# Kernel tuning notes

Measured on AMD Instinct MI355X. Metric: run time of the kernel, lower is better.

Reference implementation:

```python
import jax, jax.numpy as jnp
import numpy as np

EPS = 1e-5  # torch BatchNorm1d default eps


def _bn(h, scale, bias):
    # BatchNorm in training mode: biased variance over the node/edge dim.
    mu = h.mean(0)
    var = h.var(0)
    return (h - mu) * jax.lax.rsqrt(var + EPS) * scale + bias


def _segment_mean(msg, idx, n):
    s = jax.ops.segment_sum(msg, idx, num_segments=n)
    cnt = jax.ops.segment_sum(jnp.ones((msg.shape[0],), msg.dtype), idx, num_segments=n)
    return s / jnp.maximum(cnt, 1.0)[:, None]


def setup_inputs() -> dict:
    N, E, D, L = 50000, 800000, 64, 3
    key = jax.random.key(0)
    ks = jax.random.split(key, 7)
    return {
        "x": jax.random.normal(ks[0], (N, D), jnp.float32),
        "edge_attr": jax.random.normal(ks[1], (E, D), jnp.float32),
        "edge_index": jax.random.randint(ks[2], (2, E), 0, N, dtype=jnp.int32),
        "v_w": jax.random.normal(ks[3], (L, 4, D, D), jnp.float32) / np.sqrt(D),
        "v_b": jax.random.normal(ks[4], (L, 4, D), jnp.float32) * 0.02,
        "e_w": jax.random.normal(ks[5], (L, D, D), jnp.float32) / np.sqrt(D),
        "e_b": jax.random.normal(ks[6], (L, D), jnp.float32) * 0.02,
        "vbn_scale": jnp.ones((L, D), jnp.float32),
        "vbn_bias": jnp.zeros((L, D), jnp.float32),
        "ebn_scale": jnp.ones((L, D), jnp.float32),
        "ebn_bias": jnp.zeros((L, D), jnp.float32),
    }


def reference(x, edge_attr, edge_index, v_w, v_b, e_w, e_b,
              vbn_scale, vbn_bias, ebn_scale, ebn_bias):
    n = x.shape[0]
    dst = edge_index[0]  # aggregation target (scatter index)
    src = edge_index[1]  # neighbor node (gather index)
    num_layers = v_w.shape[0]
    w = edge_attr
    for l in range(num_layers):
        x0, w0 = x, w
        # Four node projections in one einsum: [4, N, D]
        xp = jnp.einsum('nd,kde->kne', x0, v_w[l]) + v_b[l][:, None, :]
        x1, x2, x3, x4 = xp[0], xp[1], xp[2], xp[3]
        # Anisotropic edge-gated message passing (vertex update)
        msg = jax.nn.sigmoid(w0) * x2[src]              # [E, D]
        agg = _segment_mean(msg, dst, n)                # [N, D]
        x = x0 + jax.nn.silu(_bn(x1 + agg, vbn_scale[l], vbn_bias[l]))
        # Edge update
        w1 = w0 @ e_w[l] + e_b[l]
        w = w0 + jax.nn.silu(_bn(w1 + x3[dst] + x4[src], ebn_scale[l], ebn_bias[l]))
    return x, w
```

## Files before the change

### kernel.cpp

```cpp
#include <hip/hip_runtime.h>
#include <hip/hip_bf16.h>
#include <math.h>

typedef __attribute__((ext_vector_type(8))) short bf16x8;
typedef __attribute__((ext_vector_type(4))) float f32x4;

__device__ __forceinline__ float bflo(unsigned u) { return __uint_as_float(u << 16); }
__device__ __forceinline__ float bfhi(unsigned u) { return __uint_as_float(u & 0xffff0000u); }
__device__ __forceinline__ unsigned packbf(float a, float b) {
    unsigned ua = __float_as_uint(a), ub = __float_as_uint(b);
    ua += 0x7fffu + ((ua >> 16) & 1u);
    ub += 0x7fffu + ((ub >> 16) & 1u);
    return (ua >> 16) | (ub & 0xffff0000u);
}
__device__ __forceinline__ float fsig(float w) {
    return __builtin_amdgcn_rcpf(1.f + __expf(-w));
}
__device__ __forceinline__ float silu(float g) { return g * fsig(g); }

__global__ void zero_int_kernel(int* __restrict__ p, int n) {
    int i = blockIdx.x * blockDim.x + threadIdx.x;
    int s = gridDim.x * blockDim.x;
    for (; i < n; i += s) p[i] = 0;
}

__global__ void count_kernel(const int* __restrict__ dst, int* __restrict__ cnt, int E) {
    int e = blockIdx.x * blockDim.x + threadIdx.x;
    if (e < E) atomicAdd(&cnt[dst[e]], 1);
}

__global__ __launch_bounds__(1024)
void scan_block_kernel(const int* __restrict__ cnt, int* __restrict__ off,
                       int* __restrict__ bsum, int n) {
    __shared__ int wsum[16];
    int tid = threadIdx.x, lane = tid & 63, wid = tid >> 6;
    int i = blockIdx.x * 1024 + tid;
    int v = (i < n) ? cnt[i] : 0;
    int sc = v;
    #pragma unroll
    for (int s = 1; s < 64; s <<= 1) {
        int t = __shfl_up(sc, (unsigned)s, 64);
        if (lane >= s) sc += t;
    }
    if (lane == 63) wsum[wid] = sc;
    __syncthreads();
    int woff = 0;
    for (int k = 0; k < wid; k++) woff += wsum[k];
    if (i < n) off[i + 1] = woff + sc;
    if (tid == 0) {
        int t = 0;
        #pragma unroll
        for (int k = 0; k < 16; k++) t += wsum[k];
        bsum[blockIdx.x] = t;
    }
}

__global__ void scan_tops_kernel(int* __restrict__ bsum, int nb) {
    int lane = threadIdx.x;
    int v = (lane < nb) ? bsum[lane] : 0;
    int sc = v;
    #pragma unroll
    for (int s = 1; s < 64; s <<= 1) {
        int t = __shfl_up(sc, (unsigned)s, 64);
        if (lane >= s) sc += t;
    }
    if (lane < nb) bsum[lane] = sc - v;
}

__global__ __launch_bounds__(1024)
void scan_add_kernel(int* __restrict__ off, const int* __restrict__ bsum, int n) {
    int i = blockIdx.x * 1024 + threadIdx.x;
    int b = bsum[blockIdx.x];
    if (i < n) off[i + 1] += b;
    if (i == 0) off[0] = 0;
}

__global__ void fill_csr_kernel(const int* __restrict__ dst, const int* __restrict__ src,
                                const int* __restrict__ off, int* __restrict__ cnt,
                                int* __restrict__ eidx, int* __restrict__ dstc,
                                int* __restrict__ srcc, int E) {
    int e = blockIdx.x * blockDim.x + threadIdx.x;
    if (e < E) {
        int d = dst[e];
        int pos = atomicSub(&cnt[d], 1) - 1;
        int slot = off[d] + pos;
        eidx[slot] = e;
        dstc[slot] = d;
        srcc[slot] = src[e];
    }
}

__global__ void pack_kernel(const float* __restrict__ v_w, const float* __restrict__ e_w,
                            short* __restrict__ vwp, short* __restrict__ ewp, int L) {
    int t = blockIdx.x * blockDim.x + threadIdx.x;
    if (t >= L * 5 * 4 * 2 * 64) return;
    int lane = t & 63;
    int ks = (t >> 6) & 1;
    int ft = (t >> 7) & 3;
    int mat = t >> 9;
    int layer = mat / 5, mi = mat % 5;
    const float* W = (mi < 4) ? (v_w + (long long)(layer * 4 + mi) * 4096)
                              : (e_w + (long long)layer * 4096);
    int m = ft * 16 + (lane & 15);
    int k0 = ks * 32 + (lane >> 4) * 8;
    short* dstp = (mi < 4)
        ? vwp + ((((long long)(layer * 4 + mi) * 4 + ft) * 2 + ks) * 64 + lane) * 8
        : ewp + ((((long long)layer * 4 + ft) * 2 + ks) * 64 + lane) * 8;
    #pragma unroll
    for (int j = 0; j < 8; j++) {
        unsigned u = __float_as_uint(W[(k0 + j) * 64 + m]);
        u += 0x7fffu + ((u >> 16) & 1u);
        dstp[j] = (short)(u >> 16);
    }
}

template <bool APPLY>
__global__ __launch_bounds__(256)
void node_gemm_mfma(const float* __restrict__ Xold, const float* __restrict__ h_v,
                    float* __restrict__ out_x, const float* __restrict__ fin,
                    const short* __restrict__ vwp, const float* __restrict__ vb,
                    __hip_bfloat16* __restrict__ xp, int Nn) {
    __shared__ short Xs[64 * 64];
    __shared__ short Hs[64 * 64];
    int tid = threadIdx.x;
    long long row0 = (long long)blockIdx.x * 64;

    {
        int r = tid >> 2, cq = tid & 3;
        long long row = row0 + r;
        float xv[16];
        #pragma unroll
        for (int j = 0; j < 16; j++) xv[j] = 0.f;
        if (row < Nn) {
            const float* sp = Xold + row * 64 + cq * 16;
            #pragma unroll
            for (int j = 0; j < 4; j++) {
                float4 v = *(const float4*)(sp + j * 4);
                xv[j*4] = v.x; xv[j*4+1] = v.y; xv[j*4+2] = v.z; xv[j*4+3] = v.w;
            }
            if (APPLY) {
                const float* hp = h_v + row * 64 + cq * 16;
                const float* kmp = fin + cq * 16;
                const float* kap = fin + 64 + cq * 16;
                #pragma unroll
                for (int j = 0; j < 16; j++) {
                    float g = hp[j] * kmp[j] + kap[j];
                    xv[j] = xv[j] + silu(g);
                }
                float* op = out_x + row * 64 + cq * 16;
                #pragma unroll
                for (int j = 0; j < 4; j++)
                    *(float4*)(op + j * 4) = make_float4(xv[j*4], xv[j*4+1], xv[j*4+2], xv[j*4+3]);
            }
        }
        uint4 w0, w1;
        w0.x = packbf(xv[0], xv[1]);   w0.y = packbf(xv[2], xv[3]);
        w0.z = packbf(xv[4], xv[5]);   w0.w = packbf(xv[6], xv[7]);
        w1.x = packbf(xv[8], xv[9]);   w1.y = packbf(xv[10], xv[11]);
        w1.z = packbf(xv[12], xv[13]); w1.w = packbf(xv[14], xv[15]);
        int base = r * 128 + cq * 32, swz = (r & 7) << 4;
        *(uint4*)((char*)Xs + (base ^ swz)) = w0;
        *(uint4*)((char*)Xs + ((base + 16) ^ swz)) = w1;
    }
    __syncthreads();

    int l = tid & 63;
    int rl = (tid >> 6) * 16 + (l & 15);
    bf16x8 bfr[2];
    #pragma unroll
    for (int ks = 0; ks < 2; ks++) {
        int off = (rl * 128 + ks * 64 + (l >> 4) * 16) ^ ((rl & 7) << 4);
        bfr[ks] = *(bf16x8*)((char*)Xs + off);
    }
    int q4 = (l >> 4) * 4;
    int r = tid >> 2, cc = (tid & 3) * 16;
    long long node = row0 + r;
    int swz = (r & 7) << 4;
    for (int g = 0; g < 4; g++) {
        #pragma unroll
        for (int ft = 0; ft < 4; ft++) {
            f32x4 acc = f32x4{0.f, 0.f, 0.f, 0.f};
            #pragma unroll
            for (int ks = 0; ks < 2; ks++) {
                bf16x8 a = *(const bf16x8*)(vwp + (((long long)(g * 4 + ft) * 2 + ks) * 64 + l) * 8);
                acc = __builtin_amdgcn_mfma_f32_16x16x32_bf16(a, bfr[ks], acc, 0, 0, 0);
            }
            int f0 = ft * 16 + q4;
            float4 bv = *(const float4*)&vb[g * 64 + f0];
            uint2 o;
            o.x = packbf(acc[0] + bv.x, acc[1] + bv.y);
            o.y = packbf(acc[2] + bv.z, acc[3] + bv.w);
            int hoff = (rl * 128 + f0 * 2) ^ ((rl & 7) << 4);
            *(uint2*)((char*)Hs + hoff) = o;
        }
        __syncthreads();
        if (node < Nn) {
            uint4 a = *(uint4*)((char*)Hs + ((r * 128 + cc * 2) ^ swz));
            uint4 b = *(uint4*)((char*)Hs + ((r * 128 + cc * 2 + 16) ^ swz));
            __hip_bfloat16* op = xp + ((long long)g * Nn + node) * 64 + cc;
            *(uint4*)op = a;
            *(uint4*)(op + 8) = b;
        }
        __syncthreads();
    }
}

template <bool FIRST, bool LAST>
__global__ __launch_bounds__(256)
void edge_gemm_mfma(const float* __restrict__ ea, const int* __restrict__ eidx,
                    __hip_bfloat16* __restrict__ w_csr, __hip_bfloat16* __restrict__ h_e,
                    const float* __restrict__ fin,
                    const short* __restrict__ ewp_p, const float* __restrict__ eb_p,
                    const short* __restrict__ ewp, const float* __restrict__ eb,
                    const __hip_bfloat16* __restrict__ x3p, const __hip_bfloat16* __restrict__ x4p,
                    const __hip_bfloat16* __restrict__ x3, const __hip_bfloat16* __restrict__ x4,
                    const int* __restrict__ dstc, const int* __restrict__ srcc,
                    float* __restrict__ estats) {
    __shared__ short Ws[64 * 64];
    __shared__ short Hs[64 * 68];
    __shared__ float sredS[4][64], sredQ[4][64];
    __shared__ int dstl[64], srcl[64];
    int tid = threadIdx.x;
    long long row0 = (long long)blockIdx.x * 64;

    {
        int r = tid >> 2, cq = tid & 3;
        long long grow = (row0 + r) * 64 + cq * 16;
        int base = r * 128 + cq * 32, swz = (r & 7) << 4;
        uint4 w0u, w1u;
        if (FIRST) {
            long long e0 = eidx[row0 + r];
            const float* sp = ea + e0 * 64 + cq * 16;
            float4 v0 = *(const float4*)(sp),     v1 = *(const float4*)(sp + 4);
            float4 v2 = *(const float4*)(sp + 8), v3 = *(const float4*)(sp + 12);
            w0u.x = packbf(v0.x, v0.y); w0u.y = packbf(v0.z, v0.w);
            w0u.z = packbf(v1.x, v1.y); w0u.w = packbf(v1.z, v1.w);
            w1u.x = packbf(v2.x, v2.y); w1u.y = packbf(v2.z, v2.w);
            w1u.z = packbf(v3.x, v3.y); w1u.w = packbf(v3.z, v3.w);
            *(uint4*)&w_csr[grow] = w0u;
            *(uint4*)&w_csr[grow + 8] = w1u;
        } else {
            w0u = *(const uint4*)&w_csr[grow];
            w1u = *(const uint4*)&w_csr[grow + 8];
        }
        *(uint4*)((char*)Ws + (base ^ swz)) = w0u;
        *(uint4*)((char*)Ws + ((base + 16) ^ swz)) = w1u;
        if (tid < 64) {
            dstl[tid] = dstc[row0 + tid];
            srcl[tid] = srcc[row0 + tid];
        }
    }
    __syncthreads();

    int l = tid & 63, wv = tid >> 6;
    int rl = wv * 16 + (l & 15);
    int q4 = (l >> 4) * 4;
    int rr0 = tid >> 3, rr1 = rr0 + 32;
    int c8 = (tid & 7) * 8;
    int de0 = dstl[rr0], se0 = srcl[rr0];
    int de1 = dstl[rr1], se1 = srcl[rr1];

    if (!FIRST) {
        uint4 p3a = *(const uint4*)&x3p[(long long)de0 * 64 + c8];
        uint4 p4a = *(const uint4*)&x4p[(long long)se0 * 64 + c8];
        uint4 p3b = *(const uint4*)&x3p[(long long)de1 * 64 + c8];
        uint4 p4b = *(const uint4*)&x4p[(long long)se1 * 64 + c8];

        bf16x8 bfr[2];
        #pragma unroll
        for (int ks = 0; ks < 2; ks++) {
            int off = (rl * 128 + ks * 64 + (l >> 4) * 16) ^ ((rl & 7) << 4);
            bfr[ks] = *(bf16x8*)((char*)Ws + off);
        }
        #pragma unroll
        for (int ft = 0; ft < 4; ft++) {
            f32x4 acc = f32x4{0.f, 0.f, 0.f, 0.f};
            #pragma unroll
            for (int ks = 0; ks < 2; ks++) {
                bf16x8 a = *(const bf16x8*)(ewp_p + (((long long)ft * 2 + ks) * 64 + l) * 8);
                acc = __builtin_amdgcn_mfma_f32_16x16x32_bf16(a, bfr[ks], acc, 0, 0, 0);
            }
            int f0 = ft * 16 + q4;
            float4 bv = *(const float4*)&eb_p[f0];
            uint2 o;
            o.x = packbf(acc[0] + bv.x, acc[1] + bv.y);
            o.y = packbf(acc[2] + bv.z, acc[3] + bv.w);
            *(uint2*)&Hs[rl * 68 + f0] = o;
        }
        __syncthreads();

        float4 km0 = *(const float4*)&fin[128 + c8], km1 = *(const float4*)&fin[128 + c8 + 4];
        float4 ka0 = *(const float4*)&fin[192 + c8], ka1 = *(const float4*)&fin[192 + c8 + 4];
        float kmv[8] = {km0.x, km0.y, km0.z, km0.w, km1.x, km1.y, km1.z, km1.w};
        float kav[8] = {ka0.x, ka0.y, ka0.z, ka0.w, ka1.x, ka1.y, ka1.z, ka1.w};
        #pragma unroll
        for (int p = 0; p < 2; p++) {
            int rr = p ? rr1 : rr0;
            uint4 p3 = p ? p3b : p3a;
            uint4 p4 = p ? p4b : p4a;
            unsigned u3[4] = {p3.x, p3.y, p3.z, p3.w};
            unsigned u4[4] = {p4.x, p4.y, p4.z, p4.w};
            uint4 hu = *(uint4*)&Hs[rr * 68 + c8];
            unsigned uh[4] = {hu.x, hu.y, hu.z, hu.w};
            int woff = (rr * 128 + c8 * 2) ^ ((rr & 7) << 4);
            uint4 wu = *(uint4*)((char*)Ws + woff);
            unsigned uw[4] = {wu.x, wu.y, wu.z, wu.w};
            float wn[8];
            #pragma unroll
            for (int j = 0; j < 4; j++) {
                float h0 = bflo(uh[j]) + bflo(u3[j]) + bflo(u4[j]);
                float h1 = bfhi(uh[j]) + bfhi(u3[j]) + bfhi(u4[j]);
                wn[2*j]   = bflo(uw[j]) + silu(h0 * kmv[2*j]   + kav[2*j]);
                wn[2*j+1] = bfhi(uw[j]) + silu(h1 * kmv[2*j+1] + kav[2*j+1]);
            }
            uint4 wo;
            wo.x = packbf(wn[0], wn[1]); wo.y = packbf(wn[2], wn[3]);
            wo.z = packbf(wn[4], wn[5]); wo.w = packbf(wn[6], wn[7]);
            *(uint4*)((char*)Ws + woff) = wo;
            *(uint4*)&w_csr[(row0 + rr) * 64 + c8] = wo;
        }
        __syncthreads();
    }

    uint4 g3a = *(const uint4*)&x3[(long long)de0 * 64 + c8];
    uint4 g4a = *(const uint4*)&x4[(long long)se0 * 64 + c8];
    uint4 g3b = *(const uint4*)&x3[(long long)de1 * 64 + c8];
    uint4 g4b = *(const uint4*)&x4[(long long)se1 * 64 + c8];
    bf16x8 bfr[2];
    #pragma unroll
    for (int ks = 0; ks < 2; ks++) {
        int off = (rl * 128 + ks * 64 + (l >> 4) * 16) ^ ((rl & 7) << 4);
        bfr[ks] = *(bf16x8*)((char*)Ws + off);
    }
    #pragma unroll
    for (int ft = 0; ft < 4; ft++) {
        f32x4 acc = f32x4{0.f, 0.f, 0.f, 0.f};
        #pragma unroll
        for (int ks = 0; ks < 2; ks++) {
            bf16x8 a = *(const bf16x8*)(ewp + (((long long)ft * 2 + ks) * 64 + l) * 8);
            acc = __builtin_amdgcn_mfma_f32_16x16x32_bf16(a, bfr[ks], acc, 0, 0, 0);
        }
        int f0 = ft * 16 + q4;
        float4 bv = *(const float4*)&eb[f0];
        uint2 o;
        o.x = packbf(acc[0] + bv.x, acc[1] + bv.y);
        o.y = packbf(acc[2] + bv.z, acc[3] + bv.w);
        *(uint2*)&Hs[rl * 68 + f0] = o;
    }
    __syncthreads();

    float s[8], q[8];
    #pragma unroll
    for (int j = 0; j < 8; j++) { s[j] = 0.f; q[j] = 0.f; }
    #pragma unroll
    for (int p = 0; p < 2; p++) {
        int rr = p ? rr1 : rr0;
        uint4 g3 = p ? g3b : g3a;
        uint4 g4 = p ? g4b : g4a;
        unsigned u3[4] = {g3.x, g3.y, g3.z, g3.w};
        unsigned u4[4] = {g4.x, g4.y, g4.z, g4.w};
        uint4 hu = *(uint4*)&Hs[rr * 68 + c8];
        unsigned uh[4] = {hu.x, hu.y, hu.z, hu.w};
        float h[8];
        #pragma unroll
        for (int j = 0; j < 4; j++) {
            float h0 = bflo(uh[j]) + bflo(u3[j]) + bflo(u4[j]);
            float h1 = bfhi(uh[j]) + bfhi(u3[j]) + bfhi(u4[j]);
            h[2*j] = h0; h[2*j+1] = h1;
            s[2*j] += h0; s[2*j+1] += h1;
            q[2*j] += h0 * h0; q[2*j+1] += h1 * h1;
        }
        if (LAST) {
            uint4 hv;
            hv.x = packbf(h[0], h[1]); hv.y = packbf(h[2], h[3]);
            hv.z = packbf(h[4], h[5]); hv.w = packbf(h[6], h[7]);
            *(uint4*)&h_e[(row0 + rr) * 64 + c8] = hv;
        }
    }
    #pragma unroll
    for (int d = 8; d < 64; d <<= 1) {
        #pragma unroll
        for (int j = 0; j < 8; j++) {
            s[j] += __shfl_xor(s[j], d);
            q[j] += __shfl_xor(q[j], d);
        }
    }
    if ((l >> 3) == 0) {
        #pragma unroll
        for (int j = 0; j < 8; j++) {
            sredS[wv][(l & 7) * 8 + j] = s[j];
            sredQ[wv][(l & 7) * 8 + j] = q[j];
        }
    }
    __syncthreads();
    if (tid < 128) {
        int which = tid >> 6, f = tid & 63;
        float v = which ? (sredQ[0][f] + sredQ[1][f] + sredQ[2][f] + sredQ[3][f])
                        : (sredS[0][f] + sredS[1][f] + sredS[2][f] + sredS[3][f]);
        atomicAdd(&estats[(blockIdx.x & 7) * 128 + which * 64 + f], v);
    }
}

template <bool FINAL>
__global__ __launch_bounds__(256)
void node_finish_kernel(const __hip_bfloat16* __restrict__ w_csr, const int* __restrict__ srcc,
                        const __hip_bfloat16* __restrict__ x2, const __hip_bfloat16* __restrict__ x1,
                        const int* __restrict__ off, float* __restrict__ h_v,
                        float* __restrict__ nstats,
                        const __hip_bfloat16* __restrict__ h_e, const int* __restrict__ eidx,
                        float* __restrict__ out_w, const float* __restrict__ fin, int Nn) {
    __shared__ float red[8 * 66];
    __shared__ float km[64], ka[64];
    int tid = threadIdx.x;
    if (FINAL) {
        if (tid < 64) { km[tid] = fin[128 + tid]; ka[tid] = fin[192 + tid]; }
        __syncthreads();
    }
    int hw = tid >> 5, k = tid & 31;
    int n = blockIdx.x * 8 + hw;
    float h0 = 0.f, h1 = 0.f;
    if (n < Nn) {
        int o0 = off[n], o1 = off[n + 1];
        float a0 = 0.f, a1 = 0.f;
        int j = o0;
        for (; j + 3 < o1; j += 4) {
            int s0 = srcc[j], s1 = srcc[j + 1], s2 = srcc[j + 2], s3 = srcc[j + 3];
            unsigned wu0 = *(const unsigned*)&w_csr[(long long)j * 64 + 2 * k];
            unsigned wu1 = *(const unsigned*)&w_csr[(long long)(j + 1) * 64 + 2 * k];
            unsigned wu2 = *(const unsigned*)&w_csr[(long long)(j + 2) * 64 + 2 * k];
            unsigned wu3 = *(const unsigned*)&w_csr[(long long)(j + 3) * 64 + 2 * k];
            unsigned xu0 = *(const unsigned*)&x2[(long long)s0 * 64 + 2 * k];
            unsigned xu1 = *(const unsigned*)&x2[(long long)s1 * 64 + 2 * k];
            unsigned xu2 = *(const unsigned*)&x2[(long long)s2 * 64 + 2 * k];
            unsigned xu3 = *(const unsigned*)&x2[(long long)s3 * 64 + 2 * k];
            a0 += bflo(xu0) * fsig(bflo(wu0)) + bflo(xu1) * fsig(bflo(wu1))
                + bflo(xu2) * fsig(bflo(wu2)) + bflo(xu3) * fsig(bflo(wu3));
            a1 += bfhi(xu0) * fsig(bfhi(wu0)) + bfhi(xu1) * fsig(bfhi(wu1))
                + bfhi(xu2) * fsig(bfhi(wu2)) + bfhi(xu3) * fsig(bfhi(wu3));
            if (FINAL) {
                unsigned hu0 = *(const unsigned*)&h_e[(long long)j * 64 + 2 * k];
                unsigned hu1 = *(const unsigned*)&h_e[(long long)(j + 1) * 64 + 2 * k];
                unsigned hu2 = *(const unsigned*)&h_e[(long long)(j + 2) * 64 + 2 * k];
                unsigned hu3 = *(const unsigned*)&h_e[(long long)(j + 3) * 64 + 2 * k];
                int e0 = eidx[j], e1 = eidx[j + 1], e2 = eidx[j + 2], e3 = eidx[j + 3];
                *(float2*)&out_w[(long long)e0 * 64 + 2 * k] = make_float2(
                    bflo(wu0) + silu(bflo(hu0) * km[2*k]   + ka[2*k]),
                    bfhi(wu0) + silu(bfhi(hu0) * km[2*k+1] + ka[2*k+1]));
                *(float2*)&out_w[(long long)e1 * 64 + 2 * k] = make_float2(
                    bflo(wu1) + silu(bflo(hu1) * km[2*k]   + ka[2*k]),
                    bfhi(wu1) + silu(bfhi(hu1) * km[2*k+1] + ka[2*k+1]));
                *(float2*)&out_w[(long long)e2 * 64 + 2 * k] = make_float2(
                    bflo(wu2) + silu(bflo(hu2) * km[2*k]   + ka[2*k]),
                    bfhi(wu2) + silu(bfhi(hu2) * km[2*k+1] + ka[2*k+1]));
                *(float2*)&out_w[(long long)e3 * 64 + 2 * k] = make_float2(
                    bflo(wu3) + silu(bflo(hu3) * km[2*k]   + ka[2*k]),
                    bfhi(wu3) + silu(bfhi(hu3) * km[2*k+1] + ka[2*k+1]));
            }
        }
        for (; j < o1; j++) {
            int s0 = srcc[j];
            unsigned wu0 = *(const unsigned*)&w_csr[(long long)j * 64 + 2 * k];
            unsigned xu0 = *(const unsigned*)&x2[(long long)s0 * 64 + 2 * k];
            a0 += bflo(xu0) * fsig(bflo(wu0));
            a1 += bfhi(xu0) * fsig(bfhi(wu0));
            if (FINAL) {
                unsigned hu0 = *(const unsigned*)&h_e[(long long)j * 64 + 2 * k];
                int e0 = eidx[j];
                *(float2*)&out_w[(long long)e0 * 64 + 2 * k] = make_float2(
                    bflo(wu0) + silu(bflo(hu0) * km[2*k]   + ka[2*k]),
                    bfhi(wu0) + silu(bfhi(hu0) * km[2*k+1] + ka[2*k+1]));
            }
        }
        float ic = 1.f / fmaxf((float)(o1 - o0), 1.f);
        unsigned xu = *(const unsigned*)&x1[(long long)n * 64 + 2 * k];
        h0 = bflo(xu) + a0 * ic;
        h1 = bfhi(xu) + a1 * ic;
        *(float2*)&h_v[(long long)n * 64 + 2 * k] = make_float2(h0, h1);
    }
    red[hw * 66 + 2 * k] = h0;
    red[hw * 66 + 2 * k + 1] = h1;
    __syncthreads();
    float* nst = nstats + (blockIdx.x & 7) * 128;
    if (tid < 64) {
        float s = 0.f;
        #pragma unroll
        for (int r = 0; r < 8; r++) s += red[r * 66 + tid];
        atomicAdd(&nst[tid], s);
    }
    __syncthreads();
    red[hw * 66 + 2 * k] = h0 * h0;
    red[hw * 66 + 2 * k + 1] = h1 * h1;
    __syncthreads();
    if (tid < 64) {
        float s = 0.f;
        #pragma unroll
        for (int r = 0; r < 8; r++) s += red[r * 66 + tid];
        atomicAdd(&nst[64 + tid], s);
    }
}

__global__ void finalize_edge_kernel(const float* __restrict__ estats,
                                     const float* __restrict__ es, const float* __restrict__ eb,
                                     float* __restrict__ fin, float invE) {
    int c = threadIdx.x;
    float s = 0.f, q = 0.f;
    #pragma unroll
    for (int r = 0; r < 8; r++) { s += estats[r * 128 + c]; q += estats[r * 128 + 64 + c]; }
    float mean = s * invE;
    float var = q * invE - mean * mean;
    float kmul = rsqrtf(var + 1e-5f) * es[c];
    fin[128 + c] = kmul;
    fin[192 + c] = eb[c] - mean * kmul;
}

__global__ void finalize_node_kernel(const float* __restrict__ nstats,
                                     const float* __restrict__ vs, const float* __restrict__ vb,
                                     float* __restrict__ fin, float invN) {
    int c = threadIdx.x;
    float s = 0.f, q = 0.f;
    #pragma unroll
    for (int r = 0; r < 8; r++) { s += nstats[r * 128 + c]; q += nstats[r * 128 + 64 + c]; }
    float mean = s * invN;
    float var = q * invN - mean * mean;
    float kmul = rsqrtf(var + 1e-5f) * vs[c];
    fin[c] = kmul;
    fin[64 + c] = vb[c] - mean * kmul;
}

__global__ __launch_bounds__(256)
void node_apply_kernel(const float4* __restrict__ hv4, const float4* __restrict__ xold4,
                       float4* __restrict__ out4, const float* __restrict__ fin, int total) {
    __shared__ float km[64], ka[64];
    if (threadIdx.x < 64) { km[threadIdx.x] = fin[threadIdx.x]; ka[threadIdx.x] = fin[64 + threadIdx.x]; }
    __syncthreads();
    int idx = blockIdx.x * 256 + threadIdx.x;
    if (idx >= total) return;
    int c0 = (idx & 15) * 4;
    float4 h = hv4[idx], xo = xold4[idx];
    float4 m = *(float4*)&km[c0], a = *(float4*)&ka[c0];
    float g0 = h.x * m.x + a.x, g1 = h.y * m.y + a.y, g2 = h.z * m.z + a.z, g3 = h.w * m.w + a.w;
    out4[idx] = make_float4(xo.x + silu(g0), xo.y + silu(g1),
                            xo.z + silu(g2), xo.w + silu(g3));
}

extern "C" void kernel_launch(void* const* d_in, const int* in_sizes, int n_in,
                              void* d_out, int out_size, void* d_ws, size_t ws_size,
                              hipStream_t stream) {
    const float* x_in  = (const float*)d_in[0];
    const float* ea_in = (const float*)d_in[1];
    const int*   ei    = (const int*)d_in[2];
    const float* v_w   = (const float*)d_in[3];
    const float* v_b   = (const float*)d_in[4];
    const float* e_w   = (const float*)d_in[5];
    const float* e_b   = (const float*)d_in[6];
    const float* vbn_s = (const float*)d_in[7];
    const float* vbn_b = (const float*)d_in[8];
    const float* ebn_s = (const float*)d_in[9];
    const float* ebn_b = (const float*)d_in[10];

    const int Nn = in_sizes[0] / 64;
    const int E  = in_sizes[1] / 64;
    const int L  = in_sizes[3] / (4 * 64 * 64);

    const int* dst = ei;
    const int* src = ei + E;

    float* h_v    = (float*)d_ws;
    float* nstats = h_v + (long long)Nn * 64;
    float* estats = nstats + (long long)L * 1024;
    float* fin    = estats + (long long)L * 1024;
    __hip_bfloat16* xp0   = (__hip_bfloat16*)(fin + 256);
    __hip_bfloat16* xp1   = xp0 + (long long)4 * Nn * 64;
    __hip_bfloat16* h_e   = xp1 + (long long)4 * Nn * 64;
    __hip_bfloat16* w_csr = h_e + (long long)E * 64;
    short* vwp = (short*)(w_csr + (long long)E * 64);
    short* ewp = vwp + (long long)L * 16384;
    int* cnt  = (int*)(ewp + (long long)L * 4096);
    int* off  = cnt + Nn;
    int* eidx = off + Nn + 1;
    int* dstc = eidx + E;
    int* srcc = dstc + E;
    int* bsum = srcc + E;

    size_t needed = ((size_t)Nn * 64 + (size_t)L * 2048 + 256) * 4 +
                    ((size_t)8 * Nn * 64 + (size_t)2 * E * 64 + (size_t)L * 20480) * 2 +
                    ((size_t)2 * Nn + 1 + (size_t)3 * E + 64) * 4;
    if (ws_size < needed) return;

    float* out_x = (float*)d_out;
    float* out_w = out_x + (long long)Nn * 64;

    const int nb = (Nn + 1023) / 1024;
    zero_int_kernel<<<64, 256, 0, stream>>>(cnt, Nn);
    zero_int_kernel<<<8, 256, 0, stream>>>((int*)nstats, L * 2048);
    count_kernel<<<(E + 255) / 256, 256, 0, stream>>>(dst, cnt, E);
    scan_block_kernel<<<nb, 1024, 0, stream>>>(cnt, off, bsum, Nn);
    scan_tops_kernel<<<1, 64, 0, stream>>>(bsum, nb);
    scan_add_kernel<<<nb, 1024, 0, stream>>>(off, bsum, Nn);
    fill_csr_kernel<<<(E + 255) / 256, 256, 0, stream>>>(dst, src, off, cnt, eidx, dstc, srcc, E);
    pack_kernel<<<(L * 2560 + 255) / 256, 256, 0, stream>>>(v_w, e_w, vwp, ewp, L);

    for (int l = 0; l < L; l++) {
        bool first = (l == 0);
        bool last = (l == L - 1);
        float* nst = nstats + (long long)l * 1024;
        float* est = estats + (long long)l * 1024;
        __hip_bfloat16* xp_cur  = (l & 1) ? xp1 : xp0;
        __hip_bfloat16* xp_prev = (l & 1) ? xp0 : xp1;
        const __hip_bfloat16* x1 = xp_cur;
        const __hip_bfloat16* x2 = xp_cur + (long long)Nn * 64;
        const __hip_bfloat16* x3 = xp_cur + (long long)2 * Nn * 64;
        const __hip_bfloat16* x4 = xp_cur + (long long)3 * Nn * 64;
        const __hip_bfloat16* x3p = xp_prev + (long long)2 * Nn * 64;
        const __hip_bfloat16* x4p = xp_prev + (long long)3 * Nn * 64;

        const float* xold = (l <= 1) ? x_in : out_x;
        if (first)
            node_gemm_mfma<false><<<(Nn + 63) / 64, 256, 0, stream>>>(
                x_in, h_v, out_x, fin, vwp + (long long)l * 16384, v_b + l * 256, xp_cur, Nn);
        else
            node_gemm_mfma<true><<<(Nn + 63) / 64, 256, 0, stream>>>(
                xold, h_v, out_x, fin, vwp + (long long)l * 16384, v_b + l * 256, xp_cur, Nn);

        const short* ewp_c = ewp + (long long)l * 4096;
        const short* ewp_pv = (l > 0) ? ewp + (long long)(l - 1) * 4096 : ewp_c;
        const float* eb_c = e_b + l * 64;
        const float* eb_pv = (l > 0) ? e_b + (l - 1) * 64 : eb_c;
        if (first && !last)
            edge_gemm_mfma<true, false><<<E / 64, 256, 0, stream>>>(
                ea_in, eidx, w_csr, h_e, fin, ewp_pv, eb_pv, ewp_c, eb_c,
                x3p, x4p, x3, x4, dstc, srcc, est);
        else if (first && last)
            edge_gemm_mfma<true, true><<<E / 64, 256, 0, stream>>>(
                ea_in, eidx, w_csr, h_e, fin, ewp_pv, eb_pv, ewp_c, eb_c,
                x3p, x4p, x3, x4, dstc, srcc, est);
        else if (!first && !last)
            edge_gemm_mfma<false, false><<<E / 64, 256, 0, stream>>>(
                ea_in, eidx, w_csr, h_e, fin, ewp_pv, eb_pv, ewp_c, eb_c,
                x3p, x4p, x3, x4, dstc, srcc, est);
        else
            edge_gemm_mfma<false, true><<<E / 64, 256, 0, stream>>>(
                ea_in, eidx, w_csr, h_e, fin, ewp_pv, eb_pv, ewp_c, eb_c,
                x3p, x4p, x3, x4, dstc, srcc, est);

        finalize_edge_kernel<<<1, 64, 0, stream>>>(
            est, ebn_s + l * 64, ebn_b + l * 64, fin, 1.f / (float)E);

        if (last)
            node_finish_kernel<true><<<(Nn + 7) / 8, 256, 0, stream>>>(
                w_csr, srcc, x2, x1, off, h_v, nst, h_e, eidx, out_w, fin, Nn);
        else
            node_finish_kernel<false><<<(Nn + 7) / 8, 256, 0, stream>>>(
                w_csr, srcc, x2, x1, off, h_v, nst, h_e, eidx, out_w, fin, Nn);

        finalize_node_kernel<<<1, 64, 0, stream>>>(
            nst, vbn_s + l * 64, vbn_b + l * 64, fin, 1.f / (float)Nn);

        if (last) {
            const float* xo_last = (L == 1) ? x_in : out_x;
            node_apply_kernel<<<(Nn * 16 + 255) / 256, 256, 0, stream>>>(
                (const float4*)h_v, (const float4*)xo_last, (float4*)out_x, fin, Nn * 16);
        }
    }
}
```

Measured before the change: 646.7 us.

## Fuse neighbor aggregation into edge GEMM via segmented dst reductions

Moves the sigmoid-gated message computation and per-destination summation into the edge GEMM kernel. Each edge tile is dst-sorted, so the kernel finds runs of equal dst, sums them in shared memory, and writes interior segments directly and boundary segments with atomics into a zeroed fp32 accumulator. The old CSR gather pass over w_csr and x2 becomes a light per-node mean/stats kernel, and the final out_w scatter moves to a separate streaming kernel. In exchange it adds a memset, an extra x2 gather in the edge kernel, and float atomics at tile boundaries, which make results nondeterministic.

```diff
diff --git a/kernel.cpp b/kernel.cpp
--- a/kernel.cpp
+++ b/kernel.cpp
@@ -214,12 +214,15 @@
                     const short* __restrict__ ewp, const float* __restrict__ eb,
                     const __hip_bfloat16* __restrict__ x3p, const __hip_bfloat16* __restrict__ x4p,
                     const __hip_bfloat16* __restrict__ x3, const __hip_bfloat16* __restrict__ x4,
+                    const __hip_bfloat16* __restrict__ x2,
                     const int* __restrict__ dstc, const int* __restrict__ srcc,
-                    float* __restrict__ estats) {
+                    float* __restrict__ estats, float* __restrict__ acc_buf) {
     __shared__ short Ws[64 * 64];
     __shared__ short Hs[64 * 68];
     __shared__ float sredS[4][64], sredQ[4][64];
     __shared__ int dstl[64], srcl[64];
+    __shared__ int segstart[65];
+    __shared__ int nsegS;
     int tid = threadIdx.x;
     long long row0 = (long long)blockIdx.x * 64;
 
@@ -246,8 +249,19 @@
         *(uint4*)((char*)Ws + (base ^ swz)) = w0u;
         *(uint4*)((char*)Ws + ((base + 16) ^ swz)) = w1u;
         if (tid < 64) {
-            dstl[tid] = dstc[row0 + tid];
+            int d = dstc[row0 + tid];
+            dstl[tid] = d;
             srcl[tid] = srcc[row0 + tid];
+            int dp = __shfl_up(d, 1, 64);
+            bool flag = (tid == 0) || (d != dp);
+            unsigned long long m = __ballot(flag);
+            int s = (int)__popcll(m & ((2ull << tid) - 1)) - 1;
+            if (flag) segstart[s] = tid;
+            if (tid == 63) {
+                int ns = (int)__popcll(m);
+                nsegS = ns;
+                segstart[ns] = 64;
+            }
         }
     }
     __syncthreads();
@@ -326,6 +340,8 @@
     uint4 g4a = *(const uint4*)&x4[(long long)se0 * 64 + c8];
     uint4 g3b = *(const uint4*)&x3[(long long)de1 * 64 + c8];
     uint4 g4b = *(const uint4*)&x4[(long long)se1 * 64 + c8];
+    uint4 g2a = *(const uint4*)&x2[(long long)se0 * 64 + c8];
+    uint4 g2b = *(const uint4*)&x2[(long long)se1 * 64 + c8];
     bf16x8 bfr[2];
     #pragma unroll
     for (int ks = 0; ks < 2; ks++) {
@@ -399,103 +415,121 @@
                         : (sredS[0][f] + sredS[1][f] + sredS[2][f] + sredS[3][f]);
         atomicAdd(&estats[(blockIdx.x & 7) * 128 + which * 64 + f], v);
     }
-}
-
-template <bool FINAL>
+
+    #pragma unroll
+    for (int p = 0; p < 2; p++) {
+        int rr = p ? rr1 : rr0;
+        uint4 g2 = p ? g2b : g2a;
+        unsigned u2[4] = {g2.x, g2.y, g2.z, g2.w};
+        int woff = (rr * 128 + c8 * 2) ^ ((rr & 7) << 4);
+        uint4 wu = *(uint4*)((char*)Ws + woff);
+        unsigned uw[4] = {wu.x, wu.y, wu.z, wu.w};
+        uint4 mo;
+        unsigned* mop = (unsigned*)&mo;
+        #pragma unroll
+        for (int j = 0; j < 4; j++) {
+            float m0 = bflo(u2[j]) * fsig(bflo(uw[j]));
+            float m1 = bfhi(u2[j]) * fsig(bfhi(uw[j]));
+            mop[j] = packbf(m0, m1);
+        }
+        *(uint4*)&Hs[rr * 68 + c8] = mo;
+    }
+    __syncthreads();
+
+    {
+        int fs8 = (tid & 7) * 8;
+        int nseg = nsegS;
+        for (int sg = tid >> 3; sg < nseg; sg += 32) {
+            int a = segstart[sg], b = segstart[sg + 1];
+            int node = dstl[a];
+            float sm[8] = {0.f, 0.f, 0.f, 0.f, 0.f, 0.f, 0.f, 0.f};
+            for (int r = a; r < b; r++) {
+                uint4 mu = *(uint4*)&Hs[r * 68 + fs8];
+                unsigned um[4] = {mu.x, mu.y, mu.z, mu.w};
+                #pragma unroll
+                for (int j = 0; j < 4; j++) {
+                    sm[2*j] += bflo(um[j]);
+                    sm[2*j+1] += bfhi(um[j]);
+                }
+            }
+            float* ap = acc_buf + (long long)node * 64 + fs8;
+            if (sg == 0 || sg == nseg - 1) {
+                #pragma unroll
+                for (int j = 0; j < 8; j++) atomicAdd(&ap[j], sm[j]);
+            } else {
+                *(float4*)ap       = make_float4(sm[0], sm[1], sm[2], sm[3]);
+                *(float4*)(ap + 4) = make_float4(sm[4], sm[5], sm[6], sm[7]);
+            }
+        }
+    }
+}
+
 __global__ __launch_bounds__(256)
-void node_finish_kernel(const __hip_bfloat16* __restrict__ w_csr, const int* __restrict__ srcc,
-                        const __hip_bfloat16* __restrict__ x2, const __hip_bfloat16* __restrict__ x1,
-                        const int* __restrict__ off, float* __restrict__ h_v,
-                        float* __restrict__ nstats,
-                        const __hip_bfloat16* __restrict__ h_e, const int* __restrict__ eidx,
-                        float* __restrict__ out_w, const float* __restrict__ fin, int Nn) {
-    __shared__ float red[8 * 66];
-    __shared__ float km[64], ka[64];
+void node_mean_kernel(float* __restrict__ h_v, const __hip_bfloat16* __restrict__ x1,
+                      const int* __restrict__ off, float* __restrict__ nstats, int Nn) {
+    __shared__ float red[16 * 68];
     int tid = threadIdx.x;
-    if (FINAL) {
-        if (tid < 64) { km[tid] = fin[128 + tid]; ka[tid] = fin[192 + tid]; }
-        __syncthreads();
-    }
-    int hw = tid >> 5, k = tid & 31;
-    int n = blockIdx.x * 8 + hw;
-    float h0 = 0.f, h1 = 0.f;
+    int nn = tid >> 4, c4 = (tid & 15) * 4;
+    int n = blockIdx.x * 16 + nn;
+    float h0 = 0.f, h1 = 0.f, h2 = 0.f, h3 = 0.f;
     if (n < Nn) {
-        int o0 = off[n], o1 = off[n + 1];
-        float a0 = 0.f, a1 = 0.f;
-        int j = o0;
-        for (; j + 3 < o1; j += 4) {
-            int s0 = srcc[j], s1 = srcc[j + 1], s2 = srcc[j + 2], s3 = srcc[j + 3];
-            unsigned wu0 = *(const unsigned*)&w_csr[(long long)j * 64 + 2 * k];
-            unsigned wu1 = *(const unsigned*)&w_csr[(long long)(j + 1) * 64 + 2 * k];
-            unsigned wu2 = *(const unsigned*)&w_csr[(long long)(j + 2) * 64 + 2 * k];
-            unsigned wu3 = *(const unsigned*)&w_csr[(long long)(j + 3) * 64 + 2 * k];
-            unsigned xu0 = *(const unsigned*)&x2[(long long)s0 * 64 + 2 * k];
-            unsigned xu1 = *(const unsigned*)&x2[(long long)s1 * 64 + 2 * k];
-            unsigned xu2 = *(const unsigned*)&x2[(long long)s2 * 64 + 2 * k];
-            unsigned xu3 = *(const unsigned*)&x2[(long long)s3 * 64 + 2 * k];
-            a0 += bflo(xu0) * fsig(bflo(wu0)) + bflo(xu1) * fsig(bflo(wu1))
-                + bflo(xu2) * fsig(bflo(wu2)) + bflo(xu3) * fsig(bflo(wu3));
-            a1 += bfhi(xu0) * fsig(bfhi(wu0)) + bfhi(xu1) * fsig(bfhi(wu1))
-                + bfhi(xu2) * fsig(bfhi(wu2)) + bfhi(xu3) * fsig(bfhi(wu3));
-            if (FINAL) {
-                unsigned hu0 = *(const unsigned*)&h_e[(long long)j * 64 + 2 * k];
-                unsigned hu1 = *(const unsigned*)&h_e[(long long)(j + 1) * 64 + 2 * k];
-                unsigned hu2 = *(const unsigned*)&h_e[(long long)(j + 2) * 64 + 2 * k];
-                unsigned hu3 = *(const unsigned*)&h_e[(long long)(j + 3) * 64 + 2 * k];
-                int e0 = eidx[j], e1 = eidx[j + 1], e2 = eidx[j + 2], e3 = eidx[j + 3];
-                *(float2*)&out_w[(long long)e0 * 64 + 2 * k] = make_float2(
-                    bflo(wu0) + silu(bflo(hu0) * km[2*k]   + ka[2*k]),
-                    bfhi(wu0) + silu(bfhi(hu0) * km[2*k+1] + ka[2*k+1]));
-                *(float2*)&out_w[(long long)e1 * 64 + 2 * k] = make_float2(
-                    bflo(wu1) + silu(bflo(hu1) * km[2*k]   + ka[2*k]),
-                    bfhi(wu1) + silu(bfhi(hu1) * km[2*k+1] + ka[2*k+1]));
-                *(float2*)&out_w[(long long)e2 * 64 + 2 * k] = make_float2(
-                    bflo(wu2) + silu(bflo(hu2) * km[2*k]   + ka[2*k]),
-                    bfhi(wu2) + silu(bfhi(hu2) * km[2*k+1] + ka[2*k+1]));
-                *(float2*)&out_w[(long long)e3 * 64 + 2 * k] = make_float2(
-                    bflo(wu3) + silu(bflo(hu3) * km[2*k]   + ka[2*k]),
-                    bfhi(wu3) + silu(bfhi(hu3) * km[2*k+1] + ka[2*k+1]));
-            }
-        }
-        for (; j < o1; j++) {
-            int s0 = srcc[j];
-            unsigned wu0 = *(const unsigned*)&w_csr[(long long)j * 64 + 2 * k];
-            unsigned xu0 = *(const unsigned*)&x2[(long long)s0 * 64 + 2 * k];
-            a0 += bflo(xu0) * fsig(bflo(wu0));
-            a1 += bfhi(xu0) * fsig(bfhi(wu0));
-            if (FINAL) {
-                unsigned hu0 = *(const unsigned*)&h_e[(long long)j * 64 + 2 * k];
-                int e0 = eidx[j];
-                *(float2*)&out_w[(long long)e0 * 64 + 2 * k] = make_float2(
-                    bflo(wu0) + silu(bflo(hu0) * km[2*k]   + ka[2*k]),
-                    bfhi(wu0) + silu(bfhi(hu0) * km[2*k+1] + ka[2*k+1]));
-            }
-        }
-        float ic = 1.f / fmaxf((float)(o1 - o0), 1.f);
-        unsigned xu = *(const unsigned*)&x1[(long long)n * 64 + 2 * k];
-        h0 = bflo(xu) + a0 * ic;
-        h1 = bfhi(xu) + a1 * ic;
-        *(float2*)&h_v[(long long)n * 64 + 2 * k] = make_float2(h0, h1);
-    }
-    red[hw * 66 + 2 * k] = h0;
-    red[hw * 66 + 2 * k + 1] = h1;
+        float4 a = *(float4*)&h_v[(long long)n * 64 + c4];
+        float ic = 1.f / fmaxf((float)(off[n + 1] - off[n]), 1.f);
+        uint2 xq = *(const uint2*)&x1[(long long)n * 64 + c4];
+        h0 = bflo(xq.x) + a.x * ic;
+        h1 = bfhi(xq.x) + a.y * ic;
+        h2 = bflo(xq.y) + a.z * ic;
+        h3 = bfhi(xq.y) + a.w * ic;
+        *(float4*)&h_v[(long long)n * 64 + c4] = make_float4(h0, h1, h2, h3);
+    }
+    *(float4*)&red[nn * 68 + c4] = make_float4(h0, h1, h2, h3);
     __syncthreads();
     float* nst = nstats + (blockIdx.x & 7) * 128;
     if (tid < 64) {
         float s = 0.f;
         #pragma unroll
-        for (int r = 0; r < 8; r++) s += red[r * 66 + tid];
+        for (int r = 0; r < 16; r++) s += red[r * 68 + tid];
         atomicAdd(&nst[tid], s);
     }
     __syncthreads();
-    red[hw * 66 + 2 * k] = h0 * h0;
-    red[hw * 66 + 2 * k + 1] = h1 * h1;
+    *(float4*)&red[nn * 68 + c4] = make_float4(h0 * h0, h1 * h1, h2 * h2, h3 * h3);
     __syncthreads();
     if (tid < 64) {
         float s = 0.f;
         #pragma unroll
-        for (int r = 0; r < 8; r++) s += red[r * 66 + tid];
+        for (int r = 0; r < 16; r++) s += red[r * 68 + tid];
         atomicAdd(&nst[64 + tid], s);
+    }
+}
+
+__global__ __launch_bounds__(256)
+void out_w_final_kernel(const __hip_bfloat16* __restrict__ h_e, const __hip_bfloat16* __restrict__ w_csr,
+                        const int* __restrict__ eidx, float* __restrict__ out_w,
+                        const float* __restrict__ fin, long long total8) {
+    __shared__ float km[64], ka[64];
+    if (threadIdx.x < 64) { km[threadIdx.x] = fin[128 + threadIdx.x]; ka[threadIdx.x] = fin[192 + threadIdx.x]; }
+    __syncthreads();
+    for (long long t = blockIdx.x * 256LL + threadIdx.x; t < total8; t += gridDim.x * 256LL) {
+        long long j = t >> 3;
+        int c8 = (int)(t & 7) * 8;
+        uint4 hu = *(const uint4*)&h_e[j * 64 + c8];
+        uint4 wu = *(const uint4*)&w_csr[j * 64 + c8];
+        int e = eidx[j];
+        unsigned uh[4] = {hu.x, hu.y, hu.z, hu.w};
+        unsigned uw[4] = {wu.x, wu.y, wu.z, wu.w};
+        float4 m0 = *(float4*)&km[c8], m1 = *(float4*)&km[c8 + 4];
+        float4 a0 = *(float4*)&ka[c8], a1 = *(float4*)&ka[c8 + 4];
+        float mv[8] = {m0.x, m0.y, m0.z, m0.w, m1.x, m1.y, m1.z, m1.w};
+        float av[8] = {a0.x, a0.y, a0.z, a0.w, a1.x, a1.y, a1.z, a1.w};
+        float o[8];
+        #pragma unroll
+        for (int j2 = 0; j2 < 4; j2++) {
+            o[2*j2]   = bflo(uw[j2]) + silu(bflo(uh[j2]) * mv[2*j2]   + av[2*j2]);
+            o[2*j2+1] = bfhi(uw[j2]) + silu(bfhi(uh[j2]) * mv[2*j2+1] + av[2*j2+1]);
+        }
+        float* op = out_w + (long long)e * 64 + c8;
+        *(float4*)op       = make_float4(o[0], o[1], o[2], o[3]);
+        *(float4*)(op + 4) = make_float4(o[4], o[5], o[6], o[7]);
     }
 }
 
@@ -622,6 +656,8 @@
             node_gemm_mfma<true><<<(Nn + 63) / 64, 256, 0, stream>>>(
                 xold, h_v, out_x, fin, vwp + (long long)l * 16384, v_b + l * 256, xp_cur, Nn);
 
+        hipMemsetAsync(h_v, 0, (size_t)Nn * 64 * 4, stream);
+
         const short* ewp_c = ewp + (long long)l * 4096;
         const short* ewp_pv = (l > 0) ? ewp + (long long)(l - 1) * 4096 : ewp_c;
         const float* eb_c = e_b + l * 64;
@@ -629,34 +665,32 @@
         if (first && !last)
             edge_gemm_mfma<true, false><<<E / 64, 256, 0, stream>>>(
                 ea_in, eidx, w_csr, h_e, fin, ewp_pv, eb_pv, ewp_c, eb_c,
-                x3p, x4p, x3, x4, dstc, srcc, est);
+                x3p, x4p, x3, x4, x2, dstc, srcc, est, h_v);
         else if (first && last)
             edge_gemm_mfma<true, true><<<E / 64, 256, 0, stream>>>(
                 ea_in, eidx, w_csr, h_e, fin, ewp_pv, eb_pv, ewp_c, eb_c,
-                x3p, x4p, x3, x4, dstc, srcc, est);
+                x3p, x4p, x3, x4, x2, dstc, srcc, est, h_v);
         else if (!first && !last)
             edge_gemm_mfma<false, false><<<E / 64, 256, 0, stream>>>(
                 ea_in, eidx, w_csr, h_e, fin, ewp_pv, eb_pv, ewp_c, eb_c,
-                x3p, x4p, x3, x4, dstc, srcc, est);
+                x3p, x4p, x3, x4, x2, dstc, srcc, est, h_v);
         else
             edge_gemm_mfma<false, true><<<E / 64, 256, 0, stream>>>(
                 ea_in, eidx, w_csr, h_e, fin, ewp_pv, eb_pv, ewp_c, eb_c,
-                x3p, x4p, x3, x4, dstc, srcc, est);
+                x3p, x4p, x3, x4, x2, dstc, srcc, est, h_v);
 
         finalize_edge_kernel<<<1, 64, 0, stream>>>(
             est, ebn_s + l * 64, ebn_b + l * 64, fin, 1.f / (float)E);
 
-        if (last)
-            node_finish_kernel<true><<<(Nn + 7) / 8, 256, 0, stream>>>(
-                w_csr, srcc, x2, x1, off, h_v, nst, h_e, eidx, out_w, fin, Nn);
-        else
-            node_finish_kernel<false><<<(Nn + 7) / 8, 256, 0, stream>>>(
-                w_csr, srcc, x2, x1, off, h_v, nst, h_e, eidx, out_w, fin, Nn);
+        node_mean_kernel<<<(Nn + 15) / 16, 256, 0, stream>>>(
+            h_v, x1, off, nst, Nn);
 
         finalize_node_kernel<<<1, 64, 0, stream>>>(
             nst, vbn_s + l * 64, vbn_b + l * 64, fin, 1.f / (float)Nn);
 
         if (last) {
+            out_w_final_kernel<<<4096, 256, 0, stream>>>(
+                h_e, w_csr, eidx, out_w, fin, (long long)E * 8);
             const float* xo_last = (L == 1) ? x_in : out_x;
             node_apply_kernel<<<(Nn * 16 + 255) / 256, 256, 0, stream>>>(
                 (const float4*)h_v, (const float4*)xo_last, (float4*)out_x, fin, Nn * 16);
```

Measured after the change: 740.8 us. 14.6% more time.
